# Kernel optimization log

Measured on AMD Instinct MI355X. Metric: run time of the kernel, lower is better.

Reference implementation:

```python
import jax, jax.numpy as jnp
import numpy as np

N = 100000
E = 1600000
EPS = 1e-5
NEG_SLOPE = 0.01


def _leaky(x):
    return jnp.where(x > 0, x, NEG_SLOPE * x)


def _conv2d(x, w, b):
    # x: [N,Cin,H,W], w: [Cout,Cin,kh,kw], VALID padding, stride 1
    y = jax.lax.conv_general_dilated(x, w, (1, 1), 'VALID',
                                     dimension_numbers=('NCHW', 'OIHW', 'NCHW'))
    return y + b[None, :, None, None]


def _bn(x, g, b, m, v):
    # eval-mode BatchNorm1d over feature dim
    return (x - m) * (g / jnp.sqrt(v + EPS)) + b


def setup_inputs() -> dict:
    key = jax.random.key(0)
    ks = jax.random.split(key, 64)
    d = {}
    d['inputs'] = jax.random.normal(ks[0], (N, 1, 100, 5), dtype=jnp.float32)
    d['edge_index'] = jax.random.randint(ks[1], (2, E), 0, N, dtype=jnp.int32)
    # CNN encoder params (x=10)
    d['cw1'] = 0.1 * jax.random.normal(ks[2], (10, 1, 3, 3), dtype=jnp.float32)
    d['cb1'] = jnp.zeros((10,), jnp.float32)
    d['cw2'] = 0.1 * jax.random.normal(ks[3], (20, 10, 3, 2), dtype=jnp.float32)
    d['cb2'] = jnp.zeros((20,), jnp.float32)
    d['cw3'] = 0.1 * jax.random.normal(ks[4], (1, 20, 3, 2), dtype=jnp.float32)
    d['cb3'] = jnp.zeros((1,), jnp.float32)
    dims = [94, 128, 128, 64, 64, 16]
    for i in range(5):
        fi, fo = dims[i], dims[i + 1]
        k = 8 + 4 * i
        d[f'gw{i+1}'] = jax.random.normal(ks[k], (fi, fo), jnp.float32) / np.sqrt(fi)
        d[f'gb{i+1}'] = jnp.zeros((fo,), jnp.float32)
        d[f'bn{i+1}_g'] = 1.0 + 0.1 * jax.random.normal(ks[k + 1], (fo,), jnp.float32)
        d[f'bn{i+1}_b'] = 0.1 * jax.random.normal(ks[k + 2], (fo,), jnp.float32)
        d[f'bn{i+1}_m'] = 0.1 * jax.random.normal(ks[k + 3], (fo,), jnp.float32)
        d[f'bn{i+1}_v'] = jax.random.uniform(ks[k + 3], (fo,), jnp.float32, 0.5, 1.5)
    return d


def reference(inputs, edge_index,
              cw1, cb1, cw2, cb2, cw3, cb3,
              gw1, gb1, gw2, gb2, gw3, gb3, gw4, gb4, gw5, gb5,
              bn1_g, bn1_b, bn1_m, bn1_v,
              bn2_g, bn2_b, bn2_m, bn2_v,
              bn3_g, bn3_b, bn3_m, bn3_v,
              bn4_g, bn4_b, bn4_m, bn4_v,
              bn5_g, bn5_b, bn5_m, bn5_v):
    n = inputs.shape[0]
    # --- GCN normalization (self-loops + symmetric deg^-1/2) ---
    loops = jnp.arange(n, dtype=edge_index.dtype)
    src = jnp.concatenate([edge_index[0], loops])
    dst = jnp.concatenate([edge_index[1], loops])
    deg = jax.ops.segment_sum(jnp.ones_like(src, dtype=jnp.float32), dst, num_segments=n)
    dinv = jnp.where(deg > 0, jax.lax.rsqrt(deg), 0.0)
    norm = dinv[src] * dinv[dst]  # [E+N]

    def gcn(h, w, b):
        m = (h @ w)[src] * norm[:, None]
        return jax.ops.segment_sum(m, dst, num_segments=n) + b

    # --- CNN encoder (dropout identity in eval) ---
    h = _conv2d(inputs, cw1, cb1)
    h = _leaky(h)
    h = _conv2d(h, cw2, cb2)
    h = _leaky(h)
    h = _conv2d(h, cw3, cb3)  # [N,1,94,1]
    h = jnp.tanh(h.reshape(-1, 94))

    h = jnp.tanh(_bn(gcn(h, gw1, gb1), bn1_g, bn1_b, bn1_m, bn1_v))
    h = jnp.tanh(_bn(gcn(h, gw2, gb2), bn2_g, bn2_b, bn2_m, bn2_v))
    h = jnp.tanh(_bn(gcn(h, gw3, gb3), bn3_g, bn3_b, bn3_m, bn3_v))
    h = jnp.tanh(_bn(gcn(h, gw4, gb4), bn4_g, bn4_b, bn4_m, bn4_v))
    h = _bn(gcn(h, gw5, gb5), bn5_g, bn5_b, bn5_m, bn5_v)
    return jax.nn.softmax(h, axis=1)
```

## Files before the change

### kernel.cpp

```cpp
#include <hip/hip_runtime.h>
#include <math.h>

namespace {

constexpr int NN = 100000;
constexpr int NE = 1600000;
constexpr float EPS = 1e-5f;

__device__ __forceinline__ float leaky(float x) { return fmaxf(x, 0.01f * x); }
__device__ __forceinline__ float ffma(float a, float b, float c) { return __builtin_fmaf(a, b, c); }


__global__ __launch_bounds__(256) void k_init(int* __restrict__ deg, int* __restrict__ counter, int n) {
  int i = blockIdx.x * 256 + threadIdx.x;
  if (i < n) deg[i] = 1;
  if (i == 0) counter[0] = 0;
}

__global__ __launch_bounds__(256) void k_count(const int* __restrict__ dst, int* __restrict__ deg, int e) {
  int i = blockIdx.x * 256 + threadIdx.x;
  if (i < e) atomicAdd(&deg[dst[i]], 1);
}

__global__ __launch_bounds__(256) void k_alloc(const int* __restrict__ deg, float* __restrict__ dinv,
                                               int* __restrict__ offsets, int* __restrict__ cursor,
                                               int* __restrict__ counter, int n) {
  int i = blockIdx.x * 256 + threadIdx.x;
  int lane = threadIdx.x & 63;
  int c = 0;
  if (i < n) {
    int d = deg[i];
    dinv[i] = rsqrtf((float)d);
    c = d - 1;
  }
  int v = c;
#pragma unroll
  for (int s = 1; s < 64; s <<= 1) {
    int t = __shfl_up(v, s, 64);
    if (lane >= s) v += t;
  }
  int total = __shfl(v, 63, 64);
  int base = 0;
  if (lane == 63) base = atomicAdd(counter, total);
  base = __shfl(base, 63, 64);
  if (i < n) {
    int off = base + v - c;
    offsets[i] = off;
    cursor[i] = off;
  }
}

__global__ __launch_bounds__(256) void k_fill(const int* __restrict__ src, const int* __restrict__ dst,
                                              const float* __restrict__ dinv, int* __restrict__ cursor,
                                              int2* __restrict__ adj, int e) {
  int i = blockIdx.x * 256 + threadIdx.x;
  if (i < e) {
    int s = src[i], d = dst[i];
    int p = atomicAdd(&cursor[d], 1);
    adj[p] = make_int2(s, __float_as_int(dinv[s] * dinv[d]));
  }
}

__global__ __launch_bounds__(256) void k_padw1(const float* __restrict__ gw1, float* __restrict__ w1p) {
  int i = blockIdx.x * 256 + threadIdx.x;
  if (i < 96 * 128) w1p[i] = (i < 94 * 128) ? gw1[i] : 0.f;
}

struct BNParams {
  const float* bg[5];
  const float* bv[5];
  const float* gb[5];
  const float* bm[5];
  const float* bb[5];
};
__global__ __launch_bounds__(512) void k_bnprep(BNParams p, float* __restrict__ scale, float* __restrict__ shift) {
  int i = threadIdx.x;
  if (i >= 400) return;
  const int ends[5] = {128, 256, 320, 384, 400};
  int l = 0;
  while (i >= ends[l]) l++;
  int c = i - (l ? ends[l - 1] : 0);
  float sc = p.bg[l][c] * rsqrtf(p.bv[l][c] + EPS);
  scale[i] = sc;
  shift[i] = ffma(p.gb[l][c] - p.bm[l][c], sc, p.bb[l][c]);
}

__global__ __launch_bounds__(256, 4) void k_cnn(const float* __restrict__ x,
                                             const float* __restrict__ cw1, const float* __restrict__ cb1,
                                             const float* __restrict__ cw2, const float* __restrict__ cb2,
                                             const float* __restrict__ cw3, const float* __restrict__ cb3,
                                             float* __restrict__ H) {
  __shared__ __align__(16) float inb[2][500];
  __shared__ float c1[2][2940];
  __shared__ float part[2][2][2][98];

  int tid = threadIdx.x;
  int half = tid >> 7;
  int nt = tid & 127;
  int lane = tid & 63;
  int node = blockIdx.x * 2 + half;
  int co0 = __builtin_amdgcn_readfirstlane(((tid >> 6) & 1) * 10);

  for (int i = tid; i < 2 * 2 * 2 * 98; i += 256) ((float*)part)[i] = 0.f;

  if (nt < 125) {
    const float4* xp = (const float4*)(x + (size_t)node * 500);
    ((float4*)inb[half])[nt] = xp[nt];
  }
  __syncthreads();

  {
    const float* in = inb[half];
    float* c1p = c1[half];
    int h = nt;
    if (h < 98) {
      float xv[3][5];
#pragma unroll
      for (int kh = 0; kh < 3; kh++)
#pragma unroll
        for (int c = 0; c < 5; c++) xv[kh][c] = in[(h + kh) * 5 + c];
      float* rowp = c1p + h * 3;
#pragma unroll
      for (int co = 0; co < 10; co++) {
        float b = cb1[co];
        float a0 = b, a1 = b, a2 = b;
#pragma unroll
        for (int kh = 0; kh < 3; kh++)
#pragma unroll
          for (int kw = 0; kw < 3; kw++) {
            float wv = cw1[co * 9 + kh * 3 + kw];
            a0 = ffma(xv[kh][kw + 0], wv, a0);
            a1 = ffma(xv[kh][kw + 1], wv, a1);
            a2 = ffma(xv[kh][kw + 2], wv, a2);
          }
        rowp[co * 294 + 0] = leaky(a0);
        rowp[co * 294 + 1] = leaky(a1);
        rowp[co * 294 + 2] = leaky(a2);
      }
    }
  }
  __syncthreads();

  int hg = lane >> 1, w = lane & 1;
  int h0 = hg * 3;
  float acc[3][10];
#pragma unroll
  for (int a = 0; a < 3; a++)
#pragma unroll
    for (int c = 0; c < 10; c++) acc[a][c] = 0.f;
  {
    const float* c1p = c1[half];
#pragma unroll 1
    for (int ci = 0; ci < 10; ci++) {
      float r[5][2];
      const float* base = c1p + ci * 294 + h0 * 3 + w;
#pragma unroll
      for (int i = 0; i < 5; i++) {
        r[i][0] = base[i * 3];
        r[i][1] = base[i * 3 + 1];
      }
#pragma unroll
      for (int c = 0; c < 10; c++) {
        const float* wp = cw2 + (co0 + c) * 60 + ci * 6;
        float w0 = wp[0], w1 = wp[1], w2v = wp[2], w3v = wp[3], w4 = wp[4], w5 = wp[5];
#pragma unroll
        for (int hh = 0; hh < 3; hh++) {
          float t = acc[hh][c];
          t = ffma(r[hh][0],     w0,  t);
          t = ffma(r[hh][1],     w1,  t);
          t = ffma(r[hh + 1][0], w2v, t);
          t = ffma(r[hh + 1][1], w3v, t);
          t = ffma(r[hh + 2][0], w4,  t);
          t = ffma(r[hh + 2][1], w5,  t);
          acc[hh][c] = t;
        }
      }
    }
#pragma unroll
    for (int c = 0; c < 10; c++) {
      float b = cb2[co0 + c];
#pragma unroll
      for (int hh = 0; hh < 3; hh++) acc[hh][c] = leaky(acc[hh][c] + b);
    }
  }
  __syncthreads();

  {
    float* pp = &part[half][co0 == 0 ? 0 : 1][w][0];
#pragma unroll
    for (int kh = 0; kh < 3; kh++) {
      float ws[10];
#pragma unroll
      for (int c = 0; c < 10; c++) {
        float wa = cw3[(co0 + c) * 6 + kh * 2 + 0];
        float wb = cw3[(co0 + c) * 6 + kh * 2 + 1];
        ws[c] = w ? wb : wa;
      }
#pragma unroll
      for (int hh = 0; hh < 3; hh++) {
        float s = 0.f;
#pragma unroll
        for (int c = 0; c < 10; c++) s = ffma(acc[hh][c], ws[c], s);
        pp[h0 + hh - kh + 2] += s;
      }
      __syncthreads();
    }
  }

  {
    float* Hp = H + (size_t)node * 96;
    if (nt < 94) {
      float v = part[half][0][0][nt + 2] + part[half][0][1][nt + 2]
              + part[half][1][0][nt + 2] + part[half][1][1][nt + 2] + cb3[0];
      Hp[nt] = tanhf(v);
    } else if (nt < 96) {
      Hp[nt] = 0.f;
    }
  }
}

template <int K, int FO, int BN, bool EPI = false>
__global__ __launch_bounds__(256) void k_gemm(const float* __restrict__ A, const float* __restrict__ W,
                                              float* __restrict__ C, int M,
                                              const float* __restrict__ bns = nullptr,
                                              const float* __restrict__ bnh = nullptr,
                                              int bnofs = 0) {
  __shared__ float As[64][K + 1];
  __shared__ __align__(16) float Ws[K][BN];
  int tid = threadIdx.x;
  int row_base = blockIdx.x * 64;
  int col_base = blockIdx.y * BN;

  for (int idx = tid; idx < 64 * K; idx += 256) {
    int r = idx / K, k = idx - r * K;
    int row = row_base + r;
    As[r][k] = (row < M) ? A[(size_t)row * K + k] : 0.f;
  }
  for (int idx = tid; idx < K * BN; idx += 256) {
    int r = idx / BN, c = idx - r * BN;
    Ws[r][c] = W[r * FO + col_base + c];
  }
  __syncthreads();

  if constexpr (BN == 64) {
    int ty = tid >> 4, tx = tid & 15;
    float acc[4][4] = {};
#pragma unroll 4
    for (int k = 0; k < K; k++) {
      float a0 = As[ty * 4 + 0][k];
      float a1 = As[ty * 4 + 1][k];
      float a2 = As[ty * 4 + 2][k];
      float a3 = As[ty * 4 + 3][k];
      const float4 b = *(const float4*)&Ws[k][tx * 4];
      acc[0][0] = ffma(a0, b.x, acc[0][0]); acc[0][1] = ffma(a0, b.y, acc[0][1]);
      acc[0][2] = ffma(a0, b.z, acc[0][2]); acc[0][3] = ffma(a0, b.w, acc[0][3]);
      acc[1][0] = ffma(a1, b.x, acc[1][0]); acc[1][1] = ffma(a1, b.y, acc[1][1]);
      acc[1][2] = ffma(a1, b.z, acc[1][2]); acc[1][3] = ffma(a1, b.w, acc[1][3]);
      acc[2][0] = ffma(a2, b.x, acc[2][0]); acc[2][1] = ffma(a2, b.y, acc[2][1]);
      acc[2][2] = ffma(a2, b.z, acc[2][2]); acc[2][3] = ffma(a2, b.w, acc[2][3]);
      acc[3][0] = ffma(a3, b.x, acc[3][0]); acc[3][1] = ffma(a3, b.y, acc[3][1]);
      acc[3][2] = ffma(a3, b.z, acc[3][2]); acc[3][3] = ffma(a3, b.w, acc[3][3]);
    }
    float4 s4, h4;
    if constexpr (EPI) {
      s4 = *(const float4*)&bns[bnofs + col_base + tx * 4];
      h4 = *(const float4*)&bnh[bnofs + col_base + tx * 4];
    }
#pragma unroll
    for (int i = 0; i < 4; i++) {
      int row = row_base + ty * 4 + i;
      if (row < M) {
        float4 v;
        if constexpr (EPI) {
          v.x = tanhf(ffma(acc[i][0], s4.x, h4.x));
          v.y = tanhf(ffma(acc[i][1], s4.y, h4.y));
          v.z = tanhf(ffma(acc[i][2], s4.z, h4.z));
          v.w = tanhf(ffma(acc[i][3], s4.w, h4.w));
        } else {
          v = make_float4(acc[i][0], acc[i][1], acc[i][2], acc[i][3]);
        }
        *(float4*)&C[(size_t)row * FO + col_base + tx * 4] = v;
      }
    }
  } else {
    int ty = tid >> 2, tx = tid & 3;
    float acc[4] = {};
#pragma unroll 4
    for (int k = 0; k < K; k++) {
      float a = As[ty][k];
      const float4 b = *(const float4*)&Ws[k][tx * 4];
      acc[0] = ffma(a, b.x, acc[0]); acc[1] = ffma(a, b.y, acc[1]);
      acc[2] = ffma(a, b.z, acc[2]); acc[3] = ffma(a, b.w, acc[3]);
    }
    int row = row_base + ty;
    if (row < M) *(float4*)&C[(size_t)row * FO + col_base + tx * 4] = make_float4(acc[0], acc[1], acc[2], acc[3]);
  }
}

__global__ __launch_bounds__(256) void k_agg96(const float* __restrict__ Hm,
                                               const int* __restrict__ offsets, const int* __restrict__ deg,
                                               const int2* __restrict__ adj,
                                               const float* __restrict__ dinv,
                                               float* __restrict__ out, int n) {
  int tid = threadIdx.x;
  int li = tid >> 3, c12 = (tid & 7) * 12;
  int node = blockIdx.x * 32 + li;
  if (node >= n) return;

  float dv = dinv[node];
  float se = dv * dv;
  const float4* sp = (const float4*)&Hm[(size_t)node * 96 + c12];
  float4 a0 = sp[0], a1 = sp[1], a2 = sp[2];
  a0.x *= se; a0.y *= se; a0.z *= se; a0.w *= se;
  a1.x *= se; a1.y *= se; a1.z *= se; a1.w *= se;
  a2.x *= se; a2.y *= se; a2.z *= se; a2.w *= se;

  const int2* ap = adj + offsets[node];
  int cnt = deg[node] - 1;
  int e = 0;
  for (; e + 1 < cnt; e += 2) {
    int2 e0 = ap[e], e1 = ap[e + 1];
    float n0 = __int_as_float(e0.y), n1 = __int_as_float(e1.y);
    const float4* q0 = (const float4*)&Hm[(size_t)e0.x * 96 + c12];
    const float4* q1 = (const float4*)&Hm[(size_t)e1.x * 96 + c12];
    float4 u0 = q0[0], u1 = q0[1], u2 = q0[2];
    float4 v0 = q1[0], v1 = q1[1], v2 = q1[2];
    a0.x = ffma(u0.x, n0, a0.x); a0.y = ffma(u0.y, n0, a0.y);
    a0.z = ffma(u0.z, n0, a0.z); a0.w = ffma(u0.w, n0, a0.w);
    a1.x = ffma(u1.x, n0, a1.x); a1.y = ffma(u1.y, n0, a1.y);
    a1.z = ffma(u1.z, n0, a1.z); a1.w = ffma(u1.w, n0, a1.w);
    a2.x = ffma(u2.x, n0, a2.x); a2.y = ffma(u2.y, n0, a2.y);
    a2.z = ffma(u2.z, n0, a2.z); a2.w = ffma(u2.w, n0, a2.w);
    a0.x = ffma(v0.x, n1, a0.x); a0.y = ffma(v0.y, n1, a0.y);
    a0.z = ffma(v0.z, n1, a0.z); a0.w = ffma(v0.w, n1, a0.w);
    a1.x = ffma(v1.x, n1, a1.x); a1.y = ffma(v1.y, n1, a1.y);
    a1.z = ffma(v1.z, n1, a1.z); a1.w = ffma(v1.w, n1, a1.w);
    a2.x = ffma(v2.x, n1, a2.x); a2.y = ffma(v2.y, n1, a2.y);
    a2.z = ffma(v2.z, n1, a2.z); a2.w = ffma(v2.w, n1, a2.w);
  }
  if (e < cnt) {
    int2 e0 = ap[e];
    float n0 = __int_as_float(e0.y);
    const float4* q0 = (const float4*)&Hm[(size_t)e0.x * 96 + c12];
    float4 u0 = q0[0], u1 = q0[1], u2 = q0[2];
    a0.x = ffma(u0.x, n0, a0.x); a0.y = ffma(u0.y, n0, a0.y);
    a0.z = ffma(u0.z, n0, a0.z); a0.w = ffma(u0.w, n0, a0.w);
    a1.x = ffma(u1.x, n0, a1.x); a1.y = ffma(u1.y, n0, a1.y);
    a1.z = ffma(u1.z, n0, a1.z); a1.w = ffma(u1.w, n0, a1.w);
    a2.x = ffma(u2.x, n0, a2.x); a2.y = ffma(u2.y, n0, a2.y);
    a2.z = ffma(u2.z, n0, a2.z); a2.w = ffma(u2.w, n0, a2.w);
  }
  float4* op = (float4*)&out[(size_t)node * 96 + c12];
  op[0] = a0; op[1] = a1; op[2] = a2;
}

template <int FO, bool SOFT>
__global__ __launch_bounds__(256) void k_agg(const float* __restrict__ XW,
                                             const int* __restrict__ offsets, const int* __restrict__ deg,
                                             const int2* __restrict__ adj,
                                             const float* __restrict__ dinv,
                                             const float* __restrict__ bnscale, const float* __restrict__ bnshift,
                                             int bnofs, float* __restrict__ out, int n) {
  constexpr int TPN = FO / 8;
  constexpr int NPB = 256 / TPN;
  int tid = threadIdx.x;
  int li = tid / TPN, c8 = (tid % TPN) * 8;
  int node = blockIdx.x * NPB + li;
  if (node >= n) return;

  float dv = dinv[node];
  float se = dv * dv;
  const float4* selfp = (const float4*)&XW[(size_t)node * FO + c8];
  float4 aL = selfp[0], aH = selfp[1];
  aL.x *= se; aL.y *= se; aL.z *= se; aL.w *= se;
  aH.x *= se; aH.y *= se; aH.z *= se; aH.w *= se;

  const int2* ap = adj + offsets[node];
  int cnt = deg[node] - 1;
  int e = 0;
#define EDGE_STEP(AA)                                                        \
  {                                                                          \
    float nm = __int_as_float((AA).y);                                       \
    const float4* q = (const float4*)&XW[(size_t)(AA).x * FO + c8];          \
    float4 v = q[0], w = q[1];                                               \
    aL.x = ffma(v.x, nm, aL.x); aL.y = ffma(v.y, nm, aL.y);                  \
    aL.z = ffma(v.z, nm, aL.z); aL.w = ffma(v.w, nm, aL.w);                  \
    aH.x = ffma(w.x, nm, aH.x); aH.y = ffma(w.y, nm, aH.y);                  \
    aH.z = ffma(w.z, nm, aH.z); aH.w = ffma(w.w, nm, aH.w);                  \
  }
  for (; e + 3 < cnt; e += 4) {
    int2 a0 = ap[e], a1 = ap[e + 1], a2 = ap[e + 2], a3 = ap[e + 3];
    EDGE_STEP(a0); EDGE_STEP(a1); EDGE_STEP(a2); EDGE_STEP(a3);
  }
  for (; e < cnt; e++) {
    int2 a0 = ap[e];
    EDGE_STEP(a0);
  }
#undef EDGE_STEP

  const float4 s4L = *(const float4*)&bnscale[bnofs + c8];
  const float4 s4H = *(const float4*)&bnscale[bnofs + c8 + 4];
  const float4 h4L = *(const float4*)&bnshift[bnofs + c8];
  const float4 h4H = *(const float4*)&bnshift[bnofs + c8 + 4];
  float r[8];
  r[0] = ffma(aL.x, s4L.x, h4L.x); r[1] = ffma(aL.y, s4L.y, h4L.y);
  r[2] = ffma(aL.z, s4L.z, h4L.z); r[3] = ffma(aL.w, s4L.w, h4L.w);
  r[4] = ffma(aH.x, s4H.x, h4H.x); r[5] = ffma(aH.y, s4H.y, h4H.y);
  r[6] = ffma(aH.z, s4H.z, h4H.z); r[7] = ffma(aH.w, s4H.w, h4H.w);

  float4 oL, oH;
  if constexpr (SOFT) {
    float mx = r[0];
#pragma unroll
    for (int i = 1; i < 8; i++) mx = fmaxf(mx, r[i]);
#pragma unroll
    for (int m = TPN / 2; m; m >>= 1) mx = fmaxf(mx, __shfl_xor(mx, m, TPN));
    float sm = 0.f;
#pragma unroll
    for (int i = 0; i < 8; i++) { r[i] = expf(r[i] - mx); sm += r[i]; }
#pragma unroll
    for (int m = TPN / 2; m; m >>= 1) sm += __shfl_xor(sm, m, TPN);
    float inv = 1.f / sm;
#pragma unroll
    for (int i = 0; i < 8; i++) r[i] *= inv;
  } else {
#pragma unroll
    for (int i = 0; i < 8; i++) r[i] = tanhf(r[i]);
  }
  oL = make_float4(r[0], r[1], r[2], r[3]);
  oH = make_float4(r[4], r[5], r[6], r[7]);
  float4* op = (float4*)&out[(size_t)node * FO + c8];
  op[0] = oL;
  op[1] = oH;
}

}

extern "C" void kernel_launch(void* const* d_in, const int* in_sizes, int n_in,
                              void* d_out, int out_size, void* d_ws, size_t ws_size,
                              hipStream_t stream) {
  const float* x   = (const float*)d_in[0];
  const int*   ei  = (const int*)d_in[1];
  const float* cw1 = (const float*)d_in[2];
  const float* cb1 = (const float*)d_in[3];
  const float* cw2 = (const float*)d_in[4];
  const float* cb2 = (const float*)d_in[5];
  const float* cw3 = (const float*)d_in[6];
  const float* cb3 = (const float*)d_in[7];
  const float *gw[5], *gb[5], *bng[5], *bnb[5], *bnm[5], *bnv[5];
  for (int l = 0; l < 5; l++) {
    gw[l]  = (const float*)d_in[8 + 6 * l + 0];
    gb[l]  = (const float*)d_in[8 + 6 * l + 1];
    bng[l] = (const float*)d_in[8 + 6 * l + 2];
    bnb[l] = (const float*)d_in[8 + 6 * l + 3];
    bnm[l] = (const float*)d_in[8 + 6 * l + 4];
    bnv[l] = (const float*)d_in[8 + 6 * l + 5];
  }
  const int* srcp = ei;
  const int* dstp = ei + NE;

  char* w = (char*)d_ws;
  auto alloc = [&](size_t bytes) { char* p = w; w += (bytes + 255) & ~255ULL; return p; };
  int*   deg     = (int*)alloc((size_t)NN * 4);
  int*   offsets = (int*)alloc((size_t)NN * 4);
  int*   cursor  = (int*)alloc((size_t)NN * 4);
  int*   counter = (int*)alloc(256);
  float* dinv    = (float*)alloc((size_t)NN * 4);
  int2*  adj     = (int2*)alloc((size_t)NE * 8);
  float* w1p     = (float*)alloc(96 * 128 * 4);
  float* bnscale = (float*)alloc(400 * 4);
  float* bnshift = (float*)alloc(400 * 4);
  float* bufA    = (float*)alloc((size_t)NN * 128 * 4);
  float* bufB    = (float*)alloc((size_t)NN * 128 * 4);
  float* bufC    = (float*)alloc((size_t)NN * 128 * 4);

  int nb_n = (NN + 255) / 256;
  int nb_e = (NE + 255) / 256;
  k_init<<<nb_n, 256, 0, stream>>>(deg, counter, NN);
  k_count<<<nb_e, 256, 0, stream>>>(dstp, deg, NE);
  k_alloc<<<nb_n, 256, 0, stream>>>(deg, dinv, offsets, cursor, counter, NN);
  k_fill<<<nb_e, 256, 0, stream>>>(srcp, dstp, dinv, cursor, adj, NE);
  k_padw1<<<48, 256, 0, stream>>>(gw[0], w1p);
  {
    BNParams bp;
    for (int l = 0; l < 5; l++) {
      bp.bg[l] = bng[l]; bp.bv[l] = bnv[l]; bp.gb[l] = gb[l];
      bp.bm[l] = bnm[l]; bp.bb[l] = bnb[l];
    }
    k_bnprep<<<1, 512, 0, stream>>>(bp, bnscale, bnshift);
  }

  k_cnn<<<NN / 2, 256, 0, stream>>>(x, cw1, cb1, cw2, cb2, cw3, cb3, bufA);

  int gx = (NN + 63) / 64;
  k_agg96<<<(NN + 31) / 32, 256, 0, stream>>>(bufA, offsets, deg, adj, dinv, bufB, NN);
  k_gemm<96, 128, 64, true><<<dim3(gx, 2), 256, 0, stream>>>(bufB, w1p, bufC, NN, bnscale, bnshift, 0);
  k_gemm<128, 128, 64><<<dim3(gx, 2), 256, 0, stream>>>(bufC, gw[1], bufB, NN);
  k_agg<128, false><<<(NN + 15) / 16, 256, 0, stream>>>(bufB, offsets, deg, adj, dinv,
                                                        bnscale, bnshift, 128, bufA, NN);
  k_gemm<128, 64, 64><<<dim3(gx, 1), 256, 0, stream>>>(bufA, gw[2], bufB, NN);
  k_agg<64, false><<<(NN + 31) / 32, 256, 0, stream>>>(bufB, offsets, deg, adj, dinv,
                                                       bnscale, bnshift, 256, bufC, NN);
  k_gemm<64, 64, 64><<<dim3(gx, 1), 256, 0, stream>>>(bufC, gw[3], bufB, NN);
  k_agg<64, false><<<(NN + 31) / 32, 256, 0, stream>>>(bufB, offsets, deg, adj, dinv,
                                                       bnscale, bnshift, 320, bufA, NN);
  k_gemm<64, 16, 16><<<dim3(gx, 1), 256, 0, stream>>>(bufA, gw[4], bufB, NN);
  k_agg<16, true><<<(NN + 127) / 128, 256, 0, stream>>>(bufB, offsets, deg, adj, dinv,
                                                        bnscale, bnshift, 384, (float*)d_out, NN);
}
```

Baseline: 1.398 ms.

## Sort nodes by degree to balance aggregation work across wavefronts

Adds a degree histogram, prefix scan and counting-sort scatter that build a node order grouped by in-degree. All aggregation kernels then process nodes through this order, so threads in the same wavefront have similar edge counts and less divergence. The cost is three extra small kernels with atomics. Output rows are written in scattered order, which loses the contiguous store and self-row read pattern, and atomic scatter makes node order within a bin nondeterministic.

```diff
diff --git a/kernel.cpp b/kernel.cpp
--- a/kernel.cpp
+++ b/kernel.cpp
@@ -11,10 +11,12 @@
 __device__ __forceinline__ float ffma(float a, float b, float c) { return __builtin_fmaf(a, b, c); }
 
 
-__global__ __launch_bounds__(256) void k_init(int* __restrict__ deg, int* __restrict__ counter, int n) {
+__global__ __launch_bounds__(256) void k_init(int* __restrict__ deg, int* __restrict__ counter,
+                                              int* __restrict__ bins, int n) {
   int i = blockIdx.x * 256 + threadIdx.x;
   if (i < n) deg[i] = 1;
   if (i == 0) counter[0] = 0;
+  if (blockIdx.x == 0 && threadIdx.x < 256) bins[threadIdx.x] = 0;
 }
 
 __global__ __launch_bounds__(256) void k_count(const int* __restrict__ dst, int* __restrict__ deg, int e) {
@@ -58,6 +60,30 @@
     int s = src[i], d = dst[i];
     int p = atomicAdd(&cursor[d], 1);
     adj[p] = make_int2(s, __float_as_int(dinv[s] * dinv[d]));
+  }
+}
+
+__global__ __launch_bounds__(256) void k_hist(const int* __restrict__ deg, int* __restrict__ bins, int n) {
+  int i = blockIdx.x * 256 + threadIdx.x;
+  if (i < n) atomicAdd(&bins[min(deg[i], 255)], 1);
+}
+
+__global__ __launch_bounds__(256) void k_scan(const int* __restrict__ bins, int* __restrict__ binpos) {
+  __shared__ int tmp[256];
+  int t = threadIdx.x;
+  tmp[t] = bins[t];
+  __syncthreads();
+  int acc = 0;
+  for (int i = 0; i < t; i++) acc += tmp[i];
+  binpos[t] = acc;
+}
+
+__global__ __launch_bounds__(256) void k_scatter(const int* __restrict__ deg, int* __restrict__ binpos,
+                                                 int* __restrict__ order, int n) {
+  int i = blockIdx.x * 256 + threadIdx.x;
+  if (i < n) {
+    int p = atomicAdd(&binpos[min(deg[i], 255)], 1);
+    order[p] = i;
   }
 }
 
@@ -301,11 +327,13 @@
                                                const int* __restrict__ offsets, const int* __restrict__ deg,
                                                const int2* __restrict__ adj,
                                                const float* __restrict__ dinv,
+                                               const int* __restrict__ order,
                                                float* __restrict__ out, int n) {
   int tid = threadIdx.x;
   int li = tid >> 3, c12 = (tid & 7) * 12;
-  int node = blockIdx.x * 32 + li;
-  if (node >= n) return;
+  int idx = blockIdx.x * 32 + li;
+  if (idx >= n) return;
+  int node = order[idx];
 
   float dv = dinv[node];
   float se = dv * dv;
@@ -359,14 +387,16 @@
                                              const int* __restrict__ offsets, const int* __restrict__ deg,
                                              const int2* __restrict__ adj,
                                              const float* __restrict__ dinv,
+                                             const int* __restrict__ order,
                                              const float* __restrict__ bnscale, const float* __restrict__ bnshift,
                                              int bnofs, float* __restrict__ out, int n) {
   constexpr int TPN = FO / 8;
   constexpr int NPB = 256 / TPN;
   int tid = threadIdx.x;
   int li = tid / TPN, c8 = (tid % TPN) * 8;
-  int node = blockIdx.x * NPB + li;
-  if (node >= n) return;
+  int idx = blockIdx.x * NPB + li;
+  if (idx >= n) return;
+  int node = order[idx];
 
   float dv = dinv[node];
   float se = dv * dv;
@@ -465,6 +495,9 @@
   int*   offsets = (int*)alloc((size_t)NN * 4);
   int*   cursor  = (int*)alloc((size_t)NN * 4);
   int*   counter = (int*)alloc(256);
+  int*   bins    = (int*)alloc(256 * 4);
+  int*   binpos  = (int*)alloc(256 * 4);
+  int*   order   = (int*)alloc((size_t)NN * 4);
   float* dinv    = (float*)alloc((size_t)NN * 4);
   int2*  adj     = (int2*)alloc((size_t)NE * 8);
   float* w1p     = (float*)alloc(96 * 128 * 4);
@@ -476,10 +509,13 @@
 
   int nb_n = (NN + 255) / 256;
   int nb_e = (NE + 255) / 256;
-  k_init<<<nb_n, 256, 0, stream>>>(deg, counter, NN);
+  k_init<<<nb_n, 256, 0, stream>>>(deg, counter, bins, NN);
   k_count<<<nb_e, 256, 0, stream>>>(dstp, deg, NE);
   k_alloc<<<nb_n, 256, 0, stream>>>(deg, dinv, offsets, cursor, counter, NN);
   k_fill<<<nb_e, 256, 0, stream>>>(srcp, dstp, dinv, cursor, adj, NE);
+  k_hist<<<nb_n, 256, 0, stream>>>(deg, bins, NN);
+  k_scan<<<1, 256, 0, stream>>>(bins, binpos);
+  k_scatter<<<nb_n, 256, 0, stream>>>(deg, binpos, order, NN);
   k_padw1<<<48, 256, 0, stream>>>(gw[0], w1p);
   {
     BNParams bp;
@@ -493,18 +529,18 @@
   k_cnn<<<NN / 2, 256, 0, stream>>>(x, cw1, cb1, cw2, cb2, cw3, cb3, bufA);
 
   int gx = (NN + 63) / 64;
-  k_agg96<<<(NN + 31) / 32, 256, 0, stream>>>(bufA, offsets, deg, adj, dinv, bufB, NN);
+  k_agg96<<<(NN + 31) / 32, 256, 0, stream>>>(bufA, offsets, deg, adj, dinv, order, bufB, NN);
   k_gemm<96, 128, 64, true><<<dim3(gx, 2), 256, 0, stream>>>(bufB, w1p, bufC, NN, bnscale, bnshift, 0);
   k_gemm<128, 128, 64><<<dim3(gx, 2), 256, 0, stream>>>(bufC, gw[1], bufB, NN);
-  k_agg<128, false><<<(NN + 15) / 16, 256, 0, stream>>>(bufB, offsets, deg, adj, dinv,
+  k_agg<128, false><<<(NN + 15) / 16, 256, 0, stream>>>(bufB, offsets, deg, adj, dinv, order,
                                                         bnscale, bnshift, 128, bufA, NN);
   k_gemm<128, 64, 64><<<dim3(gx, 1), 256, 0, stream>>>(bufA, gw[2], bufB, NN);
-  k_agg<64, false><<<(NN + 31) / 32, 256, 0, stream>>>(bufB, offsets, deg, adj, dinv,
+  k_agg<64, false><<<(NN + 31) / 32, 256, 0, stream>>>(bufB, offsets, deg, adj, dinv, order,
                                                        bnscale, bnshift, 256, bufC, NN);
   k_gemm<64, 64, 64><<<dim3(gx, 1), 256, 0, stream>>>(bufC, gw[3], bufB, NN);
-  k_agg<64, false><<<(NN + 31) / 32, 256, 0, stream>>>(bufB, offsets, deg, adj, dinv,
+  k_agg<64, false><<<(NN + 31) / 32, 256, 0, stream>>>(bufB, offsets, deg, adj, dinv, order,
                                                        bnscale, bnshift, 320, bufA, NN);
   k_gemm<64, 16, 16><<<dim3(gx, 1), 256, 0, stream>>>(bufA, gw[4], bufB, NN);
-  k_agg<16, true><<<(NN + 127) / 128, 256, 0, stream>>>(bufB, offsets, deg, adj, dinv,
+  k_agg<16, true><<<(NN + 127) / 128, 256, 0, stream>>>(bufB, offsets, deg, adj, dinv, order,
                                                         bnscale, bnshift, 384, (float*)d_out, NN);
 }
```

Result: slower. 1.987 ms (+42.2%).
